# Kernel tuning notes

Hardware: AMD Instinct MI355X
Metric: run time of the kernel (lower is better)

Reference implementation:

```python
import jax, jax.numpy as jnp
import numpy as np

INF = 1e10
EPS = 1e-5
B, N, F, H, NC, NRBF = 2, 512, 64, 64, 32, 50
GAMMA = 10.0  # RBF width for the continuous filter convolution kernel


def setup_inputs() -> dict:
    key = jax.random.key(0)
    ks = jax.random.split(key, 16)
    def lin(k, i, o):
        return (jax.random.normal(k, (i, o), jnp.float32) / np.sqrt(i)).astype(jnp.float32)
    d = {}
    d["h"] = jax.random.normal(ks[0], (B, N, F), jnp.float32)
    d["x"] = jax.random.normal(ks[1], (B, N, 3), jnp.float32)
    d["mask"] = jnp.ones((B, N, N), jnp.float32)
    # ContinuousFilterConvolution(2F -> H): feature branch + RBF filter branch
    d["W_dh"] = lin(ks[2], 2 * F, H); d["b_dh"] = jnp.zeros((H,), jnp.float32)
    d["mu"] = jnp.linspace(0.0, 5.0, NRBF).astype(jnp.float32)
    d["W_f"] = lin(ks[3], NRBF, H); d["b_f"] = jnp.zeros((H,), jnp.float32)
    # semantic_attention_mlp: Linear(2F,1,bias=False) + SiLU
    d["W_sa"] = lin(ks[4], 2 * F, 1)
    # edge_weight_mlp: Linear(2F+H, NC) + Tanh
    d["W_ew"] = lin(ks[5], 2 * F + H, NC); d["b_ew"] = jnp.zeros((NC,), jnp.float32)
    # post_norm_nlp: Linear(NC,H) SiLU Linear(H,H)
    d["W_pn1"] = lin(ks[6], NC, H); d["b_pn1"] = jnp.zeros((H,), jnp.float32)
    d["W_pn2"] = lin(ks[7], H, H); d["b_pn2"] = jnp.zeros((H,), jnp.float32)
    # node_mlp: Linear(2H+F,H) SiLU Linear(H,H)
    d["W_nm1"] = lin(ks[8], 2 * H + F, H); d["b_nm1"] = jnp.zeros((H,), jnp.float32)
    d["W_nm2"] = lin(ks[9], H, H); d["b_nm2"] = jnp.zeros((H,), jnp.float32)
    # coordinate_mlp: Linear(H,H) SiLU Linear(H,1)
    d["W_cm1"] = lin(ks[10], H, H); d["b_cm1"] = jnp.zeros((H,), jnp.float32)
    d["W_cm2"] = lin(ks[11], H, 1); d["b_cm2"] = jnp.zeros((1,), jnp.float32)
    return d


def reference(h, x, mask, W_dh, b_dh, mu, W_f, b_f, W_sa, W_ew, b_ew,
              W_pn1, b_pn1, W_pn2, b_pn2, W_nm1, b_nm1, W_nm2, b_nm2,
              W_cm1, b_cm1, W_cm2, b_cm2):
    silu = jax.nn.silu
    n = h.shape[-2]
    # pairwise displacements: entry [b,i,j] = x[b,j] - x[b,i]
    x_minus_xt = x[..., None, :, :] - x[..., :, None, :]                       # [B,N,N,3]
    norm = jnp.sqrt(jax.nn.relu(jnp.sum(x_minus_xt ** 2, -1, keepdims=True)) + EPS)  # [B,N,N,1]
    eye = jnp.eye(n, dtype=norm.dtype)[..., None]                              # [N,N,1]
    _norm = norm + INF * eye + (1.0 - mask[..., None]) * INF
    spatial = jax.nn.softmax(-_norm, axis=-2)                                  # softmin over senders
    # h_cat_ht[b,i,j] = concat(h[b,j], h[b,i])
    hi = jnp.broadcast_to(h[..., None, :, :], h.shape[:-2] + (n, n, h.shape[-1]))
    hj = jnp.broadcast_to(h[..., :, None, :], h.shape[:-2] + (n, n, h.shape[-1]))
    h_cat = jnp.concatenate([hi, hj], -1)                                      # [B,N,N,2F]
    # continuous filter convolution: feature MLP gated by RBF-expanded distance filter
    rbf = jnp.exp(-GAMMA * (norm - mu) ** 2)                                   # [B,N,N,NRBF]
    filtered = (h_cat @ W_dh + b_dh) * (rbf @ W_f + b_f)                       # [B,N,N,H]
    # semantic attention
    sem = silu(h_cat @ W_sa)                                                   # [B,N,N,1]
    sem = sem - INF * eye + (mask[..., None] - 1.0) * INF
    sem = jax.nn.softmax(sem, axis=-2)
    # per-edge coefficient weights on normalized displacement vectors
    w = jnp.tanh(jnp.concatenate([h_cat, filtered], -1) @ W_ew + b_ew)         # [B,N,N,NC]
    dirvec = x_minus_xt / (norm ** 2 + EPS)                                    # [B,N,N,3]
    att = w[..., None] * dirvec[..., None, :] * mask[..., None, None]          # [B,N,N,NC,3]
    att_sum = att.sum(-3)                                                      # sum over j -> [B,N,NC,3]
    att_norm = jnp.sqrt(jax.nn.relu(jnp.sum(att_sum ** 2, -1)) + EPS)          # [B,N,NC]
    emb = silu(att_norm @ W_pn1 + b_pn1) @ W_pn2 + b_pn2                       # [B,N,H]
    # edge messages and coordinate update
    h_e = filtered * mask[..., None]
    _h_e = (silu(h_e @ W_cm1 + b_cm1) @ W_cm2 + b_cm2) * mask[..., None]       # [B,N,N,1]
    _x = (x_minus_xt * _h_e).sum(-2) + x                                       # [B,N,3]
    # combined spatial*semantic attention and aggregation
    total = jax.nn.softmax(sem * spatial + (mask[..., None] - 1.0) * INF, axis=-2)
    h_e_agg = (total * h_e).sum(-2)                                            # [B,N,H]
    z = jnp.concatenate([h, h_e_agg, emb], -1)                                 # [B,N,F+2H]
    _h = silu(z @ W_nm1 + b_nm1) @ W_nm2 + b_nm2                               # [B,N,H]
    return _h, _x
```

## Files before the change

kernel.cpp:

```cpp
#include <hip/hip_runtime.h>

#define INF 1e10f
#define EPSV 1e-5f
#define NB 2
#define NN 512
#define NF 64
#define NH 64
#define NCC 32
#define NRBF 50
#define NND (NB*NN)
#define MU_STEP (5.0f/49.0f)

typedef _Float16 half8 __attribute__((ext_vector_type(8)));
typedef float f32x4 __attribute__((ext_vector_type(4)));

__device__ __forceinline__ float frcp(float x){ return __builtin_amdgcn_rcpf(x); }
__device__ __forceinline__ float silu_f(float x){ return x * frcp(1.f + __expf(-x)); }
__device__ __forceinline__ float tanh_f(float x){
  float cx = fminf(fmaxf(x, -15.f), 15.f);
  float t = __expf(2.f * cx);
  return (t - 1.f) * frcp(t + 1.f);
}

__device__ __forceinline__ float wredMax(float v){
  v = fmaxf(v, __shfl_down(v, 32)); v = fmaxf(v, __shfl_down(v, 16));
  v = fmaxf(v, __shfl_down(v, 8));  v = fmaxf(v, __shfl_down(v, 4));
  v = fmaxf(v, __shfl_down(v, 2));  v = fmaxf(v, __shfl_down(v, 1));
  return v;
}
__device__ __forceinline__ float wredSum(float v){
  v += __shfl_down(v, 32); v += __shfl_down(v, 16); v += __shfl_down(v, 8);
  v += __shfl_down(v, 4);  v += __shfl_down(v, 2);  v += __shfl_down(v, 1);
  return v;
}
__device__ __forceinline__ float bredMax(float v, float* red, int tid){
  float w = wredMax(v);
  __syncthreads();
  if ((tid & 63) == 0) red[tid >> 6] = w;
  __syncthreads();
  return fmaxf(fmaxf(red[0], red[1]), fmaxf(red[2], red[3]));
}
__device__ __forceinline__ float bredSum(float v, float* red, int tid){
  float w = wredSum(v);
  __syncthreads();
  if ((tid & 63) == 0) red[tid >> 6] = w;
  __syncthreads();
  return (red[0] + red[1]) + (red[2] + red[3]);
}

__global__ void kP(const float* __restrict__ Wf, const float* __restrict__ bf,
                   const float* __restrict__ Wcm1, const float* __restrict__ Wew,
                   unsigned int* __restrict__ frag){
  const int fi = blockIdx.x;
  const int t = threadIdx.x;
  const int lane = t >> 2, dw = t & 3;
  float v[2];
  #pragma unroll
  for (int e2 = 0; e2 < 2; ++e2){
    int e = dw * 2 + e2;
    int kk = 8 * (lane >> 4) + e;
    int n16 = lane & 15;
    float val;
    if (fi < 8){
      int mt = fi >> 1, kc = fi & 1;
      int h = 8 * (n16 >> 2) + (n16 & 3) + 4 * (mt & 1) + 32 * (mt >> 1);
      int r = kk + 32 * kc;
      val = (r < NRBF) ? Wf[r * NH + h] : ((r == NRBF) ? bf[h] : 0.f);
    } else if (fi < 16){
      int q = fi - 8; int kc = q >> 2, nt = q & 3;
      int hrow = kk + 32 * kc, kcol = n16 + 16 * nt;
      val = Wcm1[hrow * NH + kcol];
    } else {
      int q = fi - 16; int kc = q >> 1, n2 = q & 1;
      int hrow = kk + 32 * kc, nc = n16 + 16 * n2;
      val = Wew[(2 * NF + hrow) * NCC + nc];
    }
    v[e2] = val;
  }
  unsigned int lo = (unsigned int)__builtin_bit_cast(unsigned short, (_Float16)v[0]);
  unsigned int hi = (unsigned int)__builtin_bit_cast(unsigned short, (_Float16)v[1]);
  frag[fi * 256 + lane * 4 + dw] = lo | (hi << 16);
}

__global__ void kA(const float* __restrict__ h, const float* __restrict__ Wdh,
                   const float* __restrict__ Wew, const float* __restrict__ Wsa,
                   const float* __restrict__ bdh, const float* __restrict__ bew,
                   float* __restrict__ u, float* __restrict__ vb,
                   float* __restrict__ e1r, float* __restrict__ e2c,
                   float* __restrict__ s1, float* __restrict__ s2){
  const int node = blockIdx.x;
  const int l = threadIdx.x;
  __shared__ float sh[NF];
  sh[l] = h[node * NF + l];
  __syncthreads();
  float ua = 0.f, va = 0.f;
  #pragma unroll
  for (int f = 0; f < NF; ++f){
    float hv = sh[f];
    ua = fmaf(hv, Wdh[f * NH + l], ua);
    va = fmaf(hv, Wdh[(NF + f) * NH + l], va);
  }
  u[node * NH + l] = ua;
  vb[node * NH + l] = va + bdh[l];
  const int nc = l & 31;
  const int half = l >> 5;
  float ea = 0.f;
  #pragma unroll
  for (int f = 0; f < NF; ++f) ea = fmaf(sh[f], Wew[(half * NF + f) * NCC + nc], ea);
  if (half == 0) e1r[node * NCC + nc] = ea;
  else           e2c[node * NCC + nc] = ea + bew[nc];
  if (l < 2){
    const float* wp = Wsa + l * NF;
    float s = 0.f;
    #pragma unroll
    for (int f = 0; f < NF; ++f) s = fmaf(sh[f], wp[f], s);
    if (l == 0) s1[node] = s; else s2[node] = s;
  }
}

__global__ __launch_bounds__(256, 2) void kB(
    const float* __restrict__ x, const float* __restrict__ mask,
    const float* __restrict__ u, const float* __restrict__ vb,
    const float* __restrict__ s1g, const float* __restrict__ s2g,
    const float* __restrict__ e1r, const float* __restrict__ e2c,
    const float* __restrict__ Wc2, const float* __restrict__ bc1, const float* __restrict__ bc2g,
    const unsigned int* __restrict__ frag,
    float* __restrict__ hga, float* __restrict__ attn, float* __restrict__ out)
{
  const int bid = blockIdx.x;
  const int b = bid >> 9, i = bid & (NN - 1);
  const int tid = threadIdx.x;
  const int lane = tid & 63, wave = tid >> 6;
  const int l15 = lane & 15, g = lane >> 4;
  const int base = b * NN;

  __shared__ __align__(16) float4 s_geo[NN];
  __shared__ __align__(16) float4 s_c[NN];
  __shared__ float s_m[NN];
  __shared__ float s_red[4];
  __shared__ half8 s_WB[20][64];

  {
    const int4* src = (const int4*)frag;
    int4* dst = (int4*)&s_WB[0][0];
    #pragma unroll
    for (int q = 0; q < 5; ++q) dst[tid + q * 256] = src[tid + q * 256];
  }

  const float xi0 = x[(base + i) * 3 + 0];
  const float xi1 = x[(base + i) * 3 + 1];
  const float xi2 = x[(base + i) * 3 + 2];
  const float s2i = s2g[base + i];

  float aj[2], sl[2], mj[2];
  #pragma unroll
  for (int q = 0; q < 2; ++q){
    const int j = tid + q * 256;
    float d0 = x[(base + j) * 3 + 0] - xi0;
    float d1 = x[(base + j) * 3 + 1] - xi1;
    float d2 = x[(base + j) * 3 + 2] - xi2;
    float nsq = d0 * d0 + d1 * d1 + d2 * d2;
    float norm = sqrtf(fmaxf(nsq, 0.f) + EPSV);
    float m = mask[(base + i) * NN + j];
    float eye = (j == i) ? 1.f : 0.f;
    float a = -(norm + eye * INF + (1.f - m) * INF);
    float sp = s1g[base + j] + s2i;
    float sv = silu_f(sp) - eye * INF + (m - 1.f) * INF;
    s_geo[j] = make_float4(d0, d1, d2, norm);
    s_m[j] = m;
    float inv = frcp(norm * norm + EPSV) * m;
    s_c[j] = make_float4(d0 * inv, d1 * inv, d2 * inv, 0.f);
    aj[q] = a; sl[q] = sv; mj[q] = m;
  }
  float M1 = bredMax(fmaxf(aj[0], aj[1]), s_red, tid);
  float S1 = bredSum(__expf(aj[0] - M1) + __expf(aj[1] - M1), s_red, tid);
  float M2 = bredMax(fmaxf(sl[0], sl[1]), s_red, tid);
  float S2 = bredSum(__expf(sl[0] - M2) + __expf(sl[1] - M2), s_red, tid);
  const float iS1 = 1.f / S1, iS2 = 1.f / S2;
  float p[2];
  #pragma unroll
  for (int q = 0; q < 2; ++q)
    p[q] = (__expf(sl[q] - M2) * iS2) * (__expf(aj[q] - M1) * iS1) + (mj[q] - 1.f) * INF;
  float M3 = bredMax(fmaxf(p[0], p[1]), s_red, tid);
  float S3 = bredSum(__expf(p[0] - M3) + __expf(p[1] - M3), s_red, tid);
  const float iS3 = 1.f / S3;
  s_c[tid].w       = __expf(p[0] - M3) * iS3 * mj[0];
  s_c[tid + 256].w = __expf(p[1] - M3) * iS3 * mj[1];
  __syncthreads();

  float vba[16];
  {
    const float4* vp = (const float4*)(vb + (size_t)(base + i) * NH);
    float4 a0 = vp[2*g], a1 = vp[2*g+1], a2 = vp[2*g+8], a3 = vp[2*g+9];
    vba[0]=a0.x; vba[1]=a0.y; vba[2]=a0.z; vba[3]=a0.w;
    vba[4]=a1.x; vba[5]=a1.y; vba[6]=a1.z; vba[7]=a1.w;
    vba[8]=a2.x; vba[9]=a2.y; vba[10]=a2.z; vba[11]=a2.w;
    vba[12]=a3.x; vba[13]=a3.y; vba[14]=a3.z; vba[15]=a3.w;
  }
  float wc2v[4], bc1v[4];
  #pragma unroll
  for (int nt = 0; nt < 4; ++nt){ wc2v[nt] = Wc2[l15 + 16*nt]; bc1v[nt] = bc1[l15 + 16*nt]; }
  float e2v[2];
  e2v[0] = e2c[(size_t)(base + i) * NCC + l15];
  e2v[1] = e2c[(size_t)(base + i) * NCC + l15 + 16];
  const float bc2v = bc2g[0];
  const float mub0 = (float)(8 * g) * MU_STEP;
  const float mub1 = (float)(8 * g + 32) * MU_STEP;

  float hg[16];
  #pragma unroll
  for (int e = 0; e < 16; ++e) hg[e] = 0.f;
  float at[2][3] = {{0.f,0.f,0.f},{0.f,0.f,0.f}};
  float xa0 = 0.f, xa1 = 0.f, xa2 = 0.f;

  for (int jt8 = 0; jt8 < 8; ++jt8){
    const int jt = wave * 128 + jt8 * 16;
    const int jl = jt + l15;
    const float4* up = (const float4*)(u + (size_t)(base + jl) * NH);
    float4 u0 = up[2*g], u1 = up[2*g+1], u2 = up[2*g+8], u3 = up[2*g+9];
    float e1v[4][2];
    #pragma unroll
    for (int reg = 0; reg < 4; ++reg){
      const float* ep1 = e1r + (size_t)(base + jt + 4*g + reg) * NCC + l15;
      e1v[reg][0] = ep1[0]; e1v[reg][1] = ep1[16];
    }
    float normj = s_geo[jl].w;
    float tmw = s_c[jl].w;
    half8 brb[2];
    {
      float t0 = normj - mub0, t1 = normj - mub1;
      #pragma unroll
      for (int rr = 0; rr < 8; ++rr){
        float d0 = t0 - (float)rr * MU_STEP;
        float d1 = t1 - (float)rr * MU_STEP;
        float ev0 = __expf(-10.f * d0 * d0);
        float ev1 = __expf(-10.f * d1 * d1);
        int r1 = 8*g + rr + 32;
        brb[0][rr] = (_Float16)ev0;
        brb[1][rr] = (_Float16)((r1 < NRBF) ? ev1 : ((r1 == NRBF) ? 1.f : 0.f));
      }
    }
    f32x4 fc[4];
    #pragma unroll
    for (int mt = 0; mt < 4; ++mt){
      f32x4 z = {0.f,0.f,0.f,0.f};
      z = __builtin_amdgcn_mfma_f32_16x16x32_f16(s_WB[2*mt][lane],   brb[0], z, 0, 0, 0);
      z = __builtin_amdgcn_mfma_f32_16x16x32_f16(s_WB[2*mt+1][lane], brb[1], z, 0, 0, 0);
      fc[mt] = z;
    }
    float ua[16] = {u0.x,u0.y,u0.z,u0.w, u1.x,u1.y,u1.z,u1.w,
                    u2.x,u2.y,u2.z,u2.w, u3.x,u3.y,u3.z,u3.w};
    float FH[16];
    half8 afh[2];
    #pragma unroll
    for (int kc = 0; kc < 2; ++kc)
      #pragma unroll
      for (int e = 0; e < 8; ++e){
        int el = kc*8 + e;
        float f = fc[2*kc + (e>>2)][e & 3];
        FH[el] = (ua[el] + vba[el]) * f;
        afh[kc][e] = (_Float16)FH[el];
      }
    #pragma unroll
    for (int e = 0; e < 16; ++e) hg[e] = fmaf(tmw, FH[e], hg[e]);
    f32x4 cm[4];
    #pragma unroll
    for (int nt = 0; nt < 4; ++nt){
      f32x4 z = {0.f,0.f,0.f,0.f};
      z = __builtin_amdgcn_mfma_f32_16x16x32_f16(afh[0], s_WB[8+nt][lane],  z, 0, 0, 0);
      z = __builtin_amdgcn_mfma_f32_16x16x32_f16(afh[1], s_WB[12+nt][lane], z, 0, 0, 0);
      cm[nt] = z;
    }
    f32x4 ew[2];
    #pragma unroll
    for (int n2 = 0; n2 < 2; ++n2){
      f32x4 z = {0.f,0.f,0.f,0.f};
      z = __builtin_amdgcn_mfma_f32_16x16x32_f16(afh[0], s_WB[16+n2][lane], z, 0, 0, 0);
      z = __builtin_amdgcn_mfma_f32_16x16x32_f16(afh[1], s_WB[18+n2][lane], z, 0, 0, 0);
      ew[n2] = z;
    }
    float mreg[4]; float4 geo4[4], c4[4];
    #pragma unroll
    for (int reg = 0; reg < 4; ++reg){
      int jr = jt + 4*g + reg;
      mreg[reg] = s_m[jr];
      geo4[reg] = s_geo[jr];
      c4[reg]   = s_c[jr];
    }
    float hEp[4] = {0.f,0.f,0.f,0.f};
    #pragma unroll
    for (int nt = 0; nt < 4; ++nt)
      #pragma unroll
      for (int reg = 0; reg < 4; ++reg){
        float tv = silu_f(fmaf(mreg[reg], cm[nt][reg], bc1v[nt]));
        hEp[reg] = fmaf(tv, wc2v[nt], hEp[reg]);
      }
    #pragma unroll
    for (int reg = 0; reg < 4; ++reg){
      float v = hEp[reg];
      v += __shfl_xor(v, 1); v += __shfl_xor(v, 2);
      v += __shfl_xor(v, 4); v += __shfl_xor(v, 8);
      float hE = (v + bc2v) * mreg[reg];
      xa0 = fmaf(geo4[reg].x, hE, xa0);
      xa1 = fmaf(geo4[reg].y, hE, xa1);
      xa2 = fmaf(geo4[reg].z, hE, xa2);
    }
    #pragma unroll
    for (int n2 = 0; n2 < 2; ++n2)
      #pragma unroll
      for (int reg = 0; reg < 4; ++reg){
        float wv = tanh_f(ew[n2][reg] + e1v[reg][n2] + e2v[n2]);
        at[n2][0] = fmaf(wv, c4[reg].x, at[n2][0]);
        at[n2][1] = fmaf(wv, c4[reg].y, at[n2][1]);
        at[n2][2] = fmaf(wv, c4[reg].z, at[n2][2]);
      }
  }

  #pragma unroll
  for (int e = 0; e < 16; ++e){
    float v = hg[e];
    v += __shfl_xor(v, 1); v += __shfl_xor(v, 2);
    v += __shfl_xor(v, 4); v += __shfl_xor(v, 8);
    hg[e] = v;
  }
  #pragma unroll
  for (int n2 = 0; n2 < 2; ++n2)
    #pragma unroll
    for (int d = 0; d < 3; ++d){
      float v = at[n2][d];
      v += __shfl_xor(v, 16); v += __shfl_xor(v, 32);
      at[n2][d] = v;
    }
  xa0 += __shfl_xor(xa0, 16); xa0 += __shfl_xor(xa0, 32);
  xa1 += __shfl_xor(xa1, 16); xa1 += __shfl_xor(xa1, 32);
  xa2 += __shfl_xor(xa2, 16); xa2 += __shfl_xor(xa2, 32);

  __syncthreads();
  float* ep = (float*)&s_WB[0][0];
  if (l15 == 0){
    #pragma unroll
    for (int e = 0; e < 16; ++e)
      ep[wave*64 + 8*g + (e & 7) + 32*(e >> 3)] = hg[e];
  }
  if (lane < 16){
    #pragma unroll
    for (int n2 = 0; n2 < 2; ++n2)
      #pragma unroll
      for (int d = 0; d < 3; ++d)
        ep[256 + wave*96 + (l15 + 16*n2)*3 + d] = at[n2][d];
  }
  if (lane == 0){
    ep[640 + wave*3 + 0] = xa0; ep[640 + wave*3 + 1] = xa1; ep[640 + wave*3 + 2] = xa2;
  }
  __syncthreads();
  if (tid < 64)
    hga[(size_t)(base + i) * NH + tid] = ep[tid] + ep[64+tid] + ep[128+tid] + ep[192+tid];
  if (tid >= 64 && tid < 160){
    int t = tid - 64;
    ep[704 + t] = ep[256+t] + ep[352+t] + ep[448+t] + ep[544+t];
  }
  if (tid >= 192 && tid < 195){
    int d = tid - 192;
    out[NB*NN*NH + (base + i)*3 + d] =
        ep[640+d] + ep[643+d] + ep[646+d] + ep[649+d] + x[(base + i)*3 + d];
  }
  __syncthreads();
  if (tid < 32){
    float a0 = ep[704 + tid*3], a1 = ep[704 + tid*3 + 1], a2 = ep[704 + tid*3 + 2];
    attn[(size_t)(base + i) * NCC + tid] = sqrtf(fmaxf(a0*a0 + a1*a1 + a2*a2, 0.f) + EPSV);
  }
}

__global__ void kC(const float* __restrict__ h, const float* __restrict__ attn,
                   const float* __restrict__ hga,
                   const float* __restrict__ Wpn1, const float* __restrict__ bpn1,
                   const float* __restrict__ Wpn2, const float* __restrict__ bpn2,
                   const float* __restrict__ Wnm1, const float* __restrict__ bnm1,
                   const float* __restrict__ Wnm2, const float* __restrict__ bnm2,
                   float* __restrict__ out)
{
  const int node = blockIdx.x;
  const int k = threadIdx.x;
  __shared__ float sa[NCC], shh[NF], sg[NH], sq[NH], se[NH], sr[NH];
  if (k < NCC) sa[k] = attn[node * NCC + k];
  shh[k] = h[node * NF + k];
  sg[k]  = hga[node * NH + k];
  __syncthreads();
  float acc = bpn1[k];
  #pragma unroll
  for (int t = 0; t < NCC; ++t) acc = fmaf(sa[t], Wpn1[t * NH + k], acc);
  sq[k] = silu_f(acc);
  __syncthreads();
  acc = bpn2[k];
  #pragma unroll
  for (int t = 0; t < NH; ++t) acc = fmaf(sq[t], Wpn2[t * NH + k], acc);
  se[k] = acc;
  __syncthreads();
  acc = bnm1[k];
  #pragma unroll
  for (int t = 0; t < NF; ++t) acc = fmaf(shh[t], Wnm1[t * NH + k], acc);
  #pragma unroll
  for (int t = 0; t < NH; ++t) acc = fmaf(sg[t],  Wnm1[(NF + t) * NH + k], acc);
  #pragma unroll
  for (int t = 0; t < NH; ++t) acc = fmaf(se[t],  Wnm1[(NF + NH + t) * NH + k], acc);
  sr[k] = silu_f(acc);
  __syncthreads();
  acc = bnm2[k];
  #pragma unroll
  for (int t = 0; t < NH; ++t) acc = fmaf(sr[t], Wnm2[t * NH + k], acc);
  out[node * NH + k] = acc;
}

extern "C" void kernel_launch(void* const* d_in, const int* in_sizes, int n_in,
                              void* d_out, int out_size, void* d_ws, size_t ws_size,
                              hipStream_t stream){
  const float* h    = (const float*)d_in[0];
  const float* x    = (const float*)d_in[1];
  const float* mask = (const float*)d_in[2];
  const float* Wdh  = (const float*)d_in[3];
  const float* bdh  = (const float*)d_in[4];
  const float* Wf   = (const float*)d_in[6];
  const float* bf   = (const float*)d_in[7];
  const float* Wsa  = (const float*)d_in[8];
  const float* Wew  = (const float*)d_in[9];
  const float* bew  = (const float*)d_in[10];
  const float* Wpn1 = (const float*)d_in[11];
  const float* bpn1 = (const float*)d_in[12];
  const float* Wpn2 = (const float*)d_in[13];
  const float* bpn2 = (const float*)d_in[14];
  const float* Wnm1 = (const float*)d_in[15];
  const float* bnm1 = (const float*)d_in[16];
  const float* Wnm2 = (const float*)d_in[17];
  const float* bnm2 = (const float*)d_in[18];
  const float* Wcm1 = (const float*)d_in[19];
  const float* bcm1 = (const float*)d_in[20];
  const float* Wcm2 = (const float*)d_in[21];
  const float* bcm2 = (const float*)d_in[22];
  float* out = (float*)d_out;
  float* ws  = (float*)d_ws;

  float* u    = ws;
  float* vbuf = u    + 65536;
  float* s1   = vbuf + 65536;
  float* s2   = s1   + 1024;
  float* e1r  = s2   + 1024;
  float* e2c  = e1r  + 32768;
  float* hga  = e2c  + 32768;
  float* attn = hga  + 65536;
  unsigned int* fragb = (unsigned int*)(attn + 32768);

  hipLaunchKernelGGL(kP, dim3(20), dim3(256), 0, stream, Wf, bf, Wcm1, Wew, fragb);
  hipLaunchKernelGGL(kA, dim3(NND), dim3(64), 0, stream,
                     h, Wdh, Wew, Wsa, bdh, bew, u, vbuf, e1r, e2c, s1, s2);
  hipLaunchKernelGGL(kB, dim3(NND), dim3(256), 0, stream,
                     x, mask, u, vbuf, s1, s2, e1r, e2c, Wcm2, bcm1, bcm2,
                     fragb, hga, attn, out);
  hipLaunchKernelGGL(kC, dim3(NND), dim3(64), 0, stream,
                     h, attn, hga, Wpn1, bpn1, Wpn2, bpn2, Wnm1, bnm1, Wnm2, bnm2, out);
}
```

Before: 62.67 us.

## Fuse weight-prep into kA, node MLP into kB, drop softmax max passes

Folds the fp16 weight-fragment packing kernel into the first per-node kernel, which now handles four nodes per block. The final node-MLP kernel is folded into the tail of the pairwise kernel as a single-wave epilogue, so the hga/attn workspace round-trip goes away. Two kernel launches are removed. The softmax max-reduction passes are dropped and the two sum reductions are merged into one, relying on bounded exponent ranges; this cuts block barriers but risks overflow. Some MFMA B-fragments move from LDS into registers, and launch bounds rise to 3 blocks per CU, which may cause spills.

Result: slower. 113.3 us (+80.8%).

```diff
diff --git a/kernel.cpp b/kernel.cpp
--- a/kernel.cpp
+++ b/kernel.cpp
@@ -22,24 +22,11 @@
   return (t - 1.f) * frcp(t + 1.f);
 }
 
-__device__ __forceinline__ float wredMax(float v){
-  v = fmaxf(v, __shfl_down(v, 32)); v = fmaxf(v, __shfl_down(v, 16));
-  v = fmaxf(v, __shfl_down(v, 8));  v = fmaxf(v, __shfl_down(v, 4));
-  v = fmaxf(v, __shfl_down(v, 2));  v = fmaxf(v, __shfl_down(v, 1));
-  return v;
-}
 __device__ __forceinline__ float wredSum(float v){
   v += __shfl_down(v, 32); v += __shfl_down(v, 16); v += __shfl_down(v, 8);
   v += __shfl_down(v, 4);  v += __shfl_down(v, 2);  v += __shfl_down(v, 1);
   return v;
 }
-__device__ __forceinline__ float bredMax(float v, float* red, int tid){
-  float w = wredMax(v);
-  __syncthreads();
-  if ((tid & 63) == 0) red[tid >> 6] = w;
-  __syncthreads();
-  return fmaxf(fmaxf(red[0], red[1]), fmaxf(red[2], red[3]));
-}
 __device__ __forceinline__ float bredSum(float v, float* red, int tid){
   float w = wredSum(v);
   __syncthreads();
@@ -47,56 +34,34 @@
   __syncthreads();
   return (red[0] + red[1]) + (red[2] + red[3]);
 }
-
-__global__ void kP(const float* __restrict__ Wf, const float* __restrict__ bf,
-                   const float* __restrict__ Wcm1, const float* __restrict__ Wew,
-                   unsigned int* __restrict__ frag){
-  const int fi = blockIdx.x;
-  const int t = threadIdx.x;
-  const int lane = t >> 2, dw = t & 3;
-  float v[2];
-  #pragma unroll
-  for (int e2 = 0; e2 < 2; ++e2){
-    int e = dw * 2 + e2;
-    int kk = 8 * (lane >> 4) + e;
-    int n16 = lane & 15;
-    float val;
-    if (fi < 8){
-      int mt = fi >> 1, kc = fi & 1;
-      int h = 8 * (n16 >> 2) + (n16 & 3) + 4 * (mt & 1) + 32 * (mt >> 1);
-      int r = kk + 32 * kc;
-      val = (r < NRBF) ? Wf[r * NH + h] : ((r == NRBF) ? bf[h] : 0.f);
-    } else if (fi < 16){
-      int q = fi - 8; int kc = q >> 2, nt = q & 3;
-      int hrow = kk + 32 * kc, kcol = n16 + 16 * nt;
-      val = Wcm1[hrow * NH + kcol];
-    } else {
-      int q = fi - 16; int kc = q >> 1, n2 = q & 1;
-      int hrow = kk + 32 * kc, nc = n16 + 16 * n2;
-      val = Wew[(2 * NF + hrow) * NCC + nc];
-    }
-    v[e2] = val;
-  }
-  unsigned int lo = (unsigned int)__builtin_bit_cast(unsigned short, (_Float16)v[0]);
-  unsigned int hi = (unsigned int)__builtin_bit_cast(unsigned short, (_Float16)v[1]);
-  frag[fi * 256 + lane * 4 + dw] = lo | (hi << 16);
+__device__ __forceinline__ float2 bredSum2(float a, float b, float* red, int tid){
+  float wa = wredSum(a), wb = wredSum(b);
+  __syncthreads();
+  if ((tid & 63) == 0){ red[(tid >> 6) * 2] = wa; red[(tid >> 6) * 2 + 1] = wb; }
+  __syncthreads();
+  return make_float2(red[0] + red[2] + red[4] + red[6],
+                     red[1] + red[3] + red[5] + red[7]);
 }
 
 __global__ void kA(const float* __restrict__ h, const float* __restrict__ Wdh,
                    const float* __restrict__ Wew, const float* __restrict__ Wsa,
                    const float* __restrict__ bdh, const float* __restrict__ bew,
+                   const float* __restrict__ Wf, const float* __restrict__ bf,
+                   const float* __restrict__ Wcm1,
                    float* __restrict__ u, float* __restrict__ vb,
                    float* __restrict__ e1r, float* __restrict__ e2c,
-                   float* __restrict__ s1, float* __restrict__ s2){
-  const int node = blockIdx.x;
-  const int l = threadIdx.x;
-  __shared__ float sh[NF];
-  sh[l] = h[node * NF + l];
+                   float* __restrict__ s1, float* __restrict__ s2,
+                   unsigned int* __restrict__ frag){
+  const int tid = threadIdx.x;
+  const int sub = tid >> 6, l = tid & 63;
+  const int node = blockIdx.x * 4 + sub;
+  __shared__ float sh[4][NF];
+  sh[sub][l] = h[node * NF + l];
   __syncthreads();
   float ua = 0.f, va = 0.f;
   #pragma unroll
   for (int f = 0; f < NF; ++f){
-    float hv = sh[f];
+    float hv = sh[sub][f];
     ua = fmaf(hv, Wdh[f * NH + l], ua);
     va = fmaf(hv, Wdh[(NF + f) * NH + l], va);
   }
@@ -106,26 +71,59 @@
   const int half = l >> 5;
   float ea = 0.f;
   #pragma unroll
-  for (int f = 0; f < NF; ++f) ea = fmaf(sh[f], Wew[(half * NF + f) * NCC + nc], ea);
+  for (int f = 0; f < NF; ++f) ea = fmaf(sh[sub][f], Wew[(half * NF + f) * NCC + nc], ea);
   if (half == 0) e1r[node * NCC + nc] = ea;
   else           e2c[node * NCC + nc] = ea + bew[nc];
   if (l < 2){
     const float* wp = Wsa + l * NF;
     float s = 0.f;
     #pragma unroll
-    for (int f = 0; f < NF; ++f) s = fmaf(sh[f], wp[f], s);
+    for (int f = 0; f < NF; ++f) s = fmaf(sh[sub][f], wp[f], s);
     if (l == 0) s1[node] = s; else s2[node] = s;
   }
-}
-
-__global__ __launch_bounds__(256, 2) void kB(
+  if (blockIdx.x < 20){
+    const int fi = blockIdx.x;
+    const int lane = tid >> 2, dw = tid & 3;
+    float v[2];
+    #pragma unroll
+    for (int e2 = 0; e2 < 2; ++e2){
+      int e = dw * 2 + e2;
+      int kk = 8 * (lane >> 4) + e;
+      int n16 = lane & 15;
+      float val;
+      if (fi < 8){
+        int mt = fi >> 1, kc = fi & 1;
+        int hh = 8 * (n16 >> 2) + (n16 & 3) + 4 * (mt & 1) + 32 * (mt >> 1);
+        int r = kk + 32 * kc;
+        val = (r < NRBF) ? Wf[r * NH + hh] : ((r == NRBF) ? bf[hh] : 0.f);
+      } else if (fi < 16){
+        int q = fi - 8; int kc = q >> 2, nt = q & 3;
+        val = Wcm1[(kk + 32 * kc) * NH + (n16 + 16 * nt)];
+      } else {
+        int q = fi - 16; int kc = q >> 1, n2 = q & 1;
+        val = Wew[(2 * NF + kk + 32 * kc) * NCC + (n16 + 16 * n2)];
+      }
+      v[e2] = val;
+    }
+    unsigned int lo = (unsigned int)__builtin_bit_cast(unsigned short, (_Float16)v[0]);
+    unsigned int hi = (unsigned int)__builtin_bit_cast(unsigned short, (_Float16)v[1]);
+    frag[fi * 256 + lane * 4 + dw] = lo | (hi << 16);
+  }
+}
+
+__global__ __launch_bounds__(256, 3) void kB(
     const float* __restrict__ x, const float* __restrict__ mask,
+    const float* __restrict__ h_g,
     const float* __restrict__ u, const float* __restrict__ vb,
     const float* __restrict__ s1g, const float* __restrict__ s2g,
     const float* __restrict__ e1r, const float* __restrict__ e2c,
     const float* __restrict__ Wc2, const float* __restrict__ bc1, const float* __restrict__ bc2g,
     const unsigned int* __restrict__ frag,
-    float* __restrict__ hga, float* __restrict__ attn, float* __restrict__ out)
+    const float* __restrict__ Wpn1, const float* __restrict__ bpn1,
+    const float* __restrict__ Wpn2, const float* __restrict__ bpn2,
+    const float* __restrict__ Wnm1, const float* __restrict__ bnm1,
+    const float* __restrict__ Wnm2, const float* __restrict__ bnm2,
+    float* __restrict__ out)
 {
   const int bid = blockIdx.x;
   const int b = bid >> 9, i = bid & (NN - 1);
@@ -137,14 +135,22 @@
   __shared__ __align__(16) float4 s_geo[NN];
   __shared__ __align__(16) float4 s_c[NN];
   __shared__ float s_m[NN];
-  __shared__ float s_red[4];
-  __shared__ half8 s_WB[20][64];
+  __shared__ float s_red[8];
+  __shared__ half8 s_WB[8][64];
 
   {
     const int4* src = (const int4*)frag;
     int4* dst = (int4*)&s_WB[0][0];
-    #pragma unroll
-    for (int q = 0; q < 5; ++q) dst[tid + q * 256] = src[tid + q * 256];
+    dst[tid] = src[tid];
+    dst[tid + 256] = src[tid + 256];
+  }
+  half8 wc1r[8], we3r[4];
+  {
+    const int4* src = (const int4*)frag;
+    #pragma unroll
+    for (int q = 0; q < 8; ++q) wc1r[q] = __builtin_bit_cast(half8, src[(8 + q) * 64 + lane]);
+    #pragma unroll
+    for (int q = 0; q < 4; ++q) we3r[q] = __builtin_bit_cast(half8, src[(16 + q) * 64 + lane]);
   }
 
   const float xi0 = x[(base + i) * 3 + 0];
@@ -152,7 +158,7 @@
   const float xi2 = x[(base + i) * 3 + 2];
   const float s2i = s2g[base + i];
 
-  float aj[2], sl[2], mj[2];
+  float ea[2], es[2], mj[2];
   #pragma unroll
   for (int q = 0; q < 2; ++q){
     const int j = tid + q * 256;
@@ -163,29 +169,25 @@
     float norm = sqrtf(fmaxf(nsq, 0.f) + EPSV);
     float m = mask[(base + i) * NN + j];
     float eye = (j == i) ? 1.f : 0.f;
-    float a = -(norm + eye * INF + (1.f - m) * INF);
+    ea[q] = __expf(-(norm + eye * INF + (1.f - m) * INF));
     float sp = s1g[base + j] + s2i;
-    float sv = silu_f(sp) - eye * INF + (m - 1.f) * INF;
+    es[q] = __expf(silu_f(sp) - eye * INF + (m - 1.f) * INF);
     s_geo[j] = make_float4(d0, d1, d2, norm);
     s_m[j] = m;
     float inv = frcp(norm * norm + EPSV) * m;
     s_c[j] = make_float4(d0 * inv, d1 * inv, d2 * inv, 0.f);
-    aj[q] = a; sl[q] = sv; mj[q] = m;
-  }
-  float M1 = bredMax(fmaxf(aj[0], aj[1]), s_red, tid);
-  float S1 = bredSum(__expf(aj[0] - M1) + __expf(aj[1] - M1), s_red, tid);
-  float M2 = bredMax(fmaxf(sl[0], sl[1]), s_red, tid);
-  float S2 = bredSum(__expf(sl[0] - M2) + __expf(sl[1] - M2), s_red, tid);
-  const float iS1 = 1.f / S1, iS2 = 1.f / S2;
-  float p[2];
+    mj[q] = m;
+  }
+  float2 S12 = bredSum2(ea[0] + ea[1], es[0] + es[1], s_red, tid);
+  const float iS1 = 1.f / S12.x, iS2 = 1.f / S12.y;
+  float e3[2];
   #pragma unroll
   for (int q = 0; q < 2; ++q)
-    p[q] = (__expf(sl[q] - M2) * iS2) * (__expf(aj[q] - M1) * iS1) + (mj[q] - 1.f) * INF;
-  float M3 = bredMax(fmaxf(p[0], p[1]), s_red, tid);
-  float S3 = bredSum(__expf(p[0] - M3) + __expf(p[1] - M3), s_red, tid);
+    e3[q] = __expf((es[q] * iS2) * (ea[q] * iS1) + (mj[q] - 1.f) * INF);
+  float S3 = bredSum(e3[0] + e3[1], s_red, tid);
   const float iS3 = 1.f / S3;
-  s_c[tid].w       = __expf(p[0] - M3) * iS3 * mj[0];
-  s_c[tid + 256].w = __expf(p[1] - M3) * iS3 * mj[1];
+  s_c[tid].w       = e3[0] * iS3 * mj[0];
+  s_c[tid + 256].w = e3[1] * iS3 * mj[1];
   __syncthreads();
 
   float vba[16];
@@ -267,16 +269,16 @@
     #pragma unroll
     for (int nt = 0; nt < 4; ++nt){
       f32x4 z = {0.f,0.f,0.f,0.f};
-      z = __builtin_amdgcn_mfma_f32_16x16x32_f16(afh[0], s_WB[8+nt][lane],  z, 0, 0, 0);
-      z = __builtin_amdgcn_mfma_f32_16x16x32_f16(afh[1], s_WB[12+nt][lane], z, 0, 0, 0);
+      z = __builtin_amdgcn_mfma_f32_16x16x32_f16(afh[0], wc1r[nt],   z, 0, 0, 0);
+      z = __builtin_amdgcn_mfma_f32_16x16x32_f16(afh[1], wc1r[4+nt], z, 0, 0, 0);
       cm[nt] = z;
     }
     f32x4 ew[2];
     #pragma unroll
     for (int n2 = 0; n2 < 2; ++n2){
       f32x4 z = {0.f,0.f,0.f,0.f};
-      z = __builtin_amdgcn_mfma_f32_16x16x32_f16(afh[0], s_WB[16+n2][lane], z, 0, 0, 0);
-      z = __builtin_amdgcn_mfma_f32_16x16x32_f16(afh[1], s_WB[18+n2][lane], z, 0, 0, 0);
+      z = __builtin_amdgcn_mfma_f32_16x16x32_f16(afh[0], we3r[n2],   z, 0, 0, 0);
+      z = __builtin_amdgcn_mfma_f32_16x16x32_f16(afh[1], we3r[2+n2], z, 0, 0, 0);
       ew[n2] = z;
     }
     float mreg[4]; float4 geo4[4], c4[4];
@@ -354,7 +356,7 @@
   }
   __syncthreads();
   if (tid < 64)
-    hga[(size_t)(base + i) * NH + tid] = ep[tid] + ep[64+tid] + ep[128+tid] + ep[192+tid];
+    ep[832 + tid] = ep[tid] + ep[64+tid] + ep[128+tid] + ep[192+tid];
   if (tid >= 64 && tid < 160){
     int t = tid - 64;
     ep[704 + t] = ep[256+t] + ep[352+t] + ep[448+t] + ep[544+t];
@@ -367,48 +369,46 @@
   __syncthreads();
   if (tid < 32){
     float a0 = ep[704 + tid*3], a1 = ep[704 + tid*3 + 1], a2 = ep[704 + tid*3 + 2];
-    attn[(size_t)(base + i) * NCC + tid] = sqrtf(fmaxf(a0*a0 + a1*a1 + a2*a2, 0.f) + EPSV);
-  }
-}
-
-__global__ void kC(const float* __restrict__ h, const float* __restrict__ attn,
-                   const float* __restrict__ hga,
-                   const float* __restrict__ Wpn1, const float* __restrict__ bpn1,
-                   const float* __restrict__ Wpn2, const float* __restrict__ bpn2,
-                   const float* __restrict__ Wnm1, const float* __restrict__ bnm1,
-                   const float* __restrict__ Wnm2, const float* __restrict__ bnm2,
-                   float* __restrict__ out)
-{
-  const int node = blockIdx.x;
-  const int k = threadIdx.x;
-  __shared__ float sa[NCC], shh[NF], sg[NH], sq[NH], se[NH], sr[NH];
-  if (k < NCC) sa[k] = attn[node * NCC + k];
-  shh[k] = h[node * NF + k];
-  sg[k]  = hga[node * NH + k];
-  __syncthreads();
-  float acc = bpn1[k];
-  #pragma unroll
-  for (int t = 0; t < NCC; ++t) acc = fmaf(sa[t], Wpn1[t * NH + k], acc);
-  sq[k] = silu_f(acc);
-  __syncthreads();
-  acc = bpn2[k];
-  #pragma unroll
-  for (int t = 0; t < NH; ++t) acc = fmaf(sq[t], Wpn2[t * NH + k], acc);
-  se[k] = acc;
-  __syncthreads();
-  acc = bnm1[k];
-  #pragma unroll
-  for (int t = 0; t < NF; ++t) acc = fmaf(shh[t], Wnm1[t * NH + k], acc);
-  #pragma unroll
-  for (int t = 0; t < NH; ++t) acc = fmaf(sg[t],  Wnm1[(NF + t) * NH + k], acc);
-  #pragma unroll
-  for (int t = 0; t < NH; ++t) acc = fmaf(se[t],  Wnm1[(NF + NH + t) * NH + k], acc);
-  sr[k] = silu_f(acc);
-  __syncthreads();
-  acc = bnm2[k];
-  #pragma unroll
-  for (int t = 0; t < NH; ++t) acc = fmaf(sr[t], Wnm2[t * NH + k], acc);
-  out[node * NH + k] = acc;
+    ep[896 + tid] = sqrtf(fmaxf(a0*a0 + a1*a1 + a2*a2, 0.f) + EPSV);
+  }
+  __syncthreads();
+
+  if (wave == 0){
+    const int k = lane;
+    const int node = base + i;
+    ep[1056 + k] = h_g[node * NF + k];
+    asm volatile("s_waitcnt lgkmcnt(0)" ::: "memory");
+    __builtin_amdgcn_wave_barrier();
+    float acc = bpn1[k];
+    #pragma unroll
+    for (int t = 0; t < NCC; ++t) acc = fmaf(ep[896 + t], Wpn1[t * NH + k], acc);
+    ep[928 + k] = silu_f(acc);
+    asm volatile("s_waitcnt lgkmcnt(0)" ::: "memory");
+    __builtin_amdgcn_wave_barrier();
+    acc = bpn2[k];
+    #pragma unroll
+    for (int t = 0; t < NH; ++t) acc = fmaf(ep[928 + t], Wpn2[t * NH + k], acc);
+    ep[992 + k] = acc;
+    asm volatile("s_waitcnt lgkmcnt(0)" ::: "memory");
+    __builtin_amdgcn_wave_barrier();
+    acc = bnm1[k];
+    #pragma unroll
+    for (int t = 0; t < NF; ++t) acc = fmaf(ep[1056 + t], Wnm1[t * NH + k], acc);
+    #pragma unroll
+    for (int t = 0; t < NH; ++t) acc = fmaf(ep[832 + t],  Wnm1[(NF + t) * NH + k], acc);
+    #pragma unroll
+    for (int t = 0; t < NH; ++t) acc = fmaf(ep[992 + t],  Wnm1[(NF + NH + t) * NH + k], acc);
+    float srv = silu_f(acc);
+    asm volatile("s_waitcnt lgkmcnt(0)" ::: "memory");
+    __builtin_amdgcn_wave_barrier();
+    ep[928 + k] = srv;
+    asm volatile("s_waitcnt lgkmcnt(0)" ::: "memory");
+    __builtin_amdgcn_wave_barrier();
+    acc = bnm2[k];
+    #pragma unroll
+    for (int t = 0; t < NH; ++t) acc = fmaf(ep[928 + t], Wnm2[t * NH + k], acc);
+    out[node * NH + k] = acc;
+  }
 }
 
 extern "C" void kernel_launch(void* const* d_in, const int* in_sizes, int n_in,
@@ -445,16 +445,13 @@
   float* s2   = s1   + 1024;
   float* e1r  = s2   + 1024;
   float* e2c  = e1r  + 32768;
-  float* hga  = e2c  + 32768;
-  float* attn = hga  + 65536;
-  unsigned int* fragb = (unsigned int*)(attn + 32768);
-
-  hipLaunchKernelGGL(kP, dim3(20), dim3(256), 0, stream, Wf, bf, Wcm1, Wew, fragb);
-  hipLaunchKernelGGL(kA, dim3(NND), dim3(64), 0, stream,
-                     h, Wdh, Wew, Wsa, bdh, bew, u, vbuf, e1r, e2c, s1, s2);
+  unsigned int* fragb = (unsigned int*)(e2c + 32768);
+
+  hipLaunchKernelGGL(kA, dim3(NND / 4), dim3(256), 0, stream,
+                     h, Wdh, Wew, Wsa, bdh, bew, Wf, bf, Wcm1,
+                     u, vbuf, e1r, e2c, s1, s2, fragb);
   hipLaunchKernelGGL(kB, dim3(NND), dim3(256), 0, stream,
-                     x, mask, u, vbuf, s1, s2, e1r, e2c, Wcm2, bcm1, bcm2,
-                     fragb, hga, attn, out);
-  hipLaunchKernelGGL(kC, dim3(NND), dim3(64), 0, stream,
-                     h, attn, hga, Wpn1, bpn1, Wpn2, bpn2, Wnm1, bnm1, Wnm2, bnm2, out);
-}
+                     x, mask, h, u, vbuf, s1, s2, e1r, e2c,
+                     Wcm2, bcm1, bcm2, fragb,
+                     Wpn1, bpn1, Wpn2, bpn2, Wnm1, bnm1, Wnm2, bnm2, out);
+}
```
